# Kernel optimization log

Measured on AMD Instinct MI355X. Metric: run time of the kernel, lower is better.

The kernel has to match this reference:

```python
import jax, jax.numpy as jnp
import numpy as np

EPS = 1e-12

def gcn_layer(x, W, row, col, vals, n_nodes):
    # support = x @ W ; out = relu(spmm(adj, support)) with adj in COO form
    support = x @ W                                  # [N, out]
    msgs = vals[:, None] * support[col]              # [E, out] gather
    agg = jax.ops.segment_sum(msgs, row, num_segments=n_nodes)
    return jax.nn.relu(agg)

def l2norm(x):
    return x / jnp.maximum(jnp.linalg.norm(x, axis=1, keepdims=True), EPS)

def setup_inputs() -> dict:
    key = jax.random.key(0)
    ks = jax.random.split(key, 16)
    N, D, A, Da, E = 20000, 1000, 1000, 100, 160000
    inp = {
        'emb_sr': jax.random.normal(ks[0], (N, D), jnp.float32) * 0.02,
        'emb_tg': jax.random.normal(ks[1], (N, D), jnp.float32) * 0.02,
        'attr_weight_sr': jax.random.uniform(ks[2], (N, A), jnp.float32),
        'attr_weight_tg': jax.random.uniform(ks[3], (N, A), jnp.float32),
        'row_sr': jax.random.randint(ks[4], (E,), 0, N, jnp.int32),
        'col_sr': jax.random.randint(ks[5], (E,), 0, N, jnp.int32),
        'vals_sr': jax.random.uniform(ks[6], (E,), jnp.float32),
        'row_tg': jax.random.randint(ks[7], (E,), 0, N, jnp.int32),
        'col_tg': jax.random.randint(ks[8], (E,), 0, N, jnp.int32),
        'vals_tg': jax.random.uniform(ks[9], (E,), jnp.float32),
        'W_s0': jax.random.normal(ks[10], (D, D), jnp.float32) * (1.0 / np.sqrt(D)),
        'W_s1': jax.random.normal(ks[11], (D, D), jnp.float32) * (1.0 / np.sqrt(D)),
        'W_a11': jax.random.normal(ks[12], (A, Da), jnp.float32) * (1.0 / np.sqrt(A)),
        'W_a12': jax.random.normal(ks[13], (A, Da), jnp.float32) * (1.0 / np.sqrt(A)),
        'W_a2': jax.random.normal(ks[14], (Da, Da), jnp.float32) * (1.0 / np.sqrt(Da)),
    }
    return inp

def reference(emb_sr, emb_tg, attr_weight_sr, attr_weight_tg,
              row_sr, col_sr, vals_sr, row_tg, col_tg, vals_tg,
              W_s0, W_s1, W_a11, W_a12, W_a2):
    N = emb_sr.shape[0]
    M = emb_tg.shape[0]
    # structural branch: 2 shared GCN layers over each graph
    sr = emb_sr
    tg = emb_tg
    for W in (W_s0, W_s1):
        sr = gcn_layer(sr, W, row_sr, col_sr, vals_sr, N)
        tg = gcn_layer(tg, W, row_tg, col_tg, vals_tg, M)
    sr = l2norm(sr)
    tg = l2norm(tg)
    # attribute branch
    sr_a = gcn_layer(attr_weight_sr, W_a11, row_sr, col_sr, vals_sr, N)
    sr_a = gcn_layer(sr_a, W_a2, row_sr, col_sr, vals_sr, N)
    tg_a = gcn_layer(attr_weight_tg, W_a12, row_tg, col_tg, vals_tg, M)
    tg_a = gcn_layer(tg_a, W_a2, row_tg, col_tg, vals_tg, M)
    return (sr, tg, sr_a, tg_a)
```

## Files before the change

kernel.cpp:

```cpp
#include <hip/hip_runtime.h>

#define N_NODES 20000
#define D_IN    1000
#define E_EDGES 160000
#define DA      100

#define MPAD 20224
#define DP   1024
#define DAP  128
#define MBLK 157
#define NRB  1250
#define PEMAX (E_EDGES + 4 * N_NODES)

typedef __bf16 bf16x8 __attribute__((ext_vector_type(8)));
typedef float  f32x4  __attribute__((ext_vector_type(4)));
typedef short  short8v __attribute__((ext_vector_type(8)));

__device__ __forceinline__ short f2bf(float f) {
  __bf16 h = (__bf16)f;
  return *(short*)&h;
}
__device__ __forceinline__ float bf2f(short s) {
  return __uint_as_float(((unsigned)(unsigned short)s) << 16);
}

#define GLDS16(g, l) __builtin_amdgcn_global_load_lds( \
    (const __attribute__((address_space(1))) void*)(g), \
    (__attribute__((address_space(3))) void*)(l), 16, 0, 0)


__global__ void cvt_pad4_v3(const float* __restrict__ s0, const float* __restrict__ s1,
                            const float* __restrict__ s2, const float* __restrict__ s3,
                            short* __restrict__ d0, short* __restrict__ d1,
                            short* __restrict__ d2, short* __restrict__ d3) {
  const float* src; short* dst;
  switch (blockIdx.z) {
    case 0:  src = s0; dst = d0; break;
    case 1:  src = s1; dst = d1; break;
    case 2:  src = s2; dst = d2; break;
    default: src = s3; dst = d3; break;
  }
  const int lane = threadIdx.x & 63;
  const int r = blockIdx.y * 4 + (threadIdx.x >> 6);
  const int u1 = lane + 64;
  short8v o0 = {0, 0, 0, 0, 0, 0, 0, 0};
  short8v o1 = {0, 0, 0, 0, 0, 0, 0, 0};
  if (r < N_NODES) {
    const float* p0 = src + (size_t)r * D_IN + lane * 8;
    float4 a0 = *(const float4*)p0;
    float4 a1 = *(const float4*)(p0 + 4);
    o0[0] = f2bf(a0.x); o0[1] = f2bf(a0.y); o0[2] = f2bf(a0.z); o0[3] = f2bf(a0.w);
    o0[4] = f2bf(a1.x); o0[5] = f2bf(a1.y); o0[6] = f2bf(a1.z); o0[7] = f2bf(a1.w);
    if (u1 < 125) {
      const float* p1 = src + (size_t)r * D_IN + u1 * 8;
      float4 b0 = *(const float4*)p1;
      float4 b1 = *(const float4*)(p1 + 4);
      o1[0] = f2bf(b0.x); o1[1] = f2bf(b0.y); o1[2] = f2bf(b0.z); o1[3] = f2bf(b0.w);
      o1[4] = f2bf(b1.x); o1[5] = f2bf(b1.y); o1[6] = f2bf(b1.z); o1[7] = f2bf(b1.w);
    }
  }
  *(short8v*)&dst[(size_t)r * DP + lane * 8] = o0;
  *(short8v*)&dst[(size_t)r * DP + u1 * 8] = o1;
}

__global__ void cvt_w_t2_k(const float* __restrict__ s0, const float* __restrict__ s1,
                           int K, int Nc,
                           short* __restrict__ d0, short* __restrict__ d1, int Kp) {
  const float* src = blockIdx.z ? s1 : s0;
  short* dst = blockIdx.z ? d1 : d0;
  int n = blockIdx.y;
  int k = blockIdx.x * blockDim.x + threadIdx.x;
  if (k >= Kp) return;
  float v = (k < K && n < Nc) ? src[(size_t)k * Nc + n] : 0.f;
  dst[(size_t)n * Kp + k] = f2bf(v);
}

__global__ void zero_int_k(int* p, int n) {
  int i = blockIdx.x * blockDim.x + threadIdx.x;
  if (i < n) p[i] = 0;
}


__global__ void hist2_k(const int* __restrict__ row0, const int* __restrict__ row1, int E,
                        int* __restrict__ deg0, int* __restrict__ deg1) {
  int e = blockIdx.x * blockDim.x + threadIdx.x;
  if (e < E) atomicAdd(&deg0[row0[e]], 1);
  else if (e < 2 * E) atomicAdd(&deg1[row1[e - E]], 1);
}

#define SCAN_T 1024
#define SCAN_C 20
__launch_bounds__(SCAN_T)
__global__ void scan_pad2_k(const int* __restrict__ dg0, const int* __restrict__ dg1, int n,
                            int* __restrict__ p0, int* __restrict__ p1) {
  const int* deg = blockIdx.x ? dg1 : dg0;
  int* poffs = blockIdx.x ? p1 : p0;
  __shared__ int lds[SCAN_T];
  int t = threadIdx.x;
  int base = t * SCAN_C;
  int v[SCAN_C];
  int s = 0;
#pragma unroll
  for (int i = 0; i < SCAN_C; ++i) {
    int idx = base + i;
    int x = (idx < n) ? ((deg[idx] + 3) & ~3) : 0;
    s += x;
    v[i] = s;
  }
  lds[t] = s;
  __syncthreads();
  for (int off = 1; off < SCAN_T; off <<= 1) {
    int add = (t >= off) ? lds[t - off] : 0;
    __syncthreads();
    lds[t] += add;
    __syncthreads();
  }
  int prefix = lds[t] - s;
#pragma unroll
  for (int i = 0; i < SCAN_C; ++i) {
    int idx = base + i;
    if (idx < n) poffs[idx + 1] = v[i] + prefix;
  }
  if (t == 0) poffs[0] = 0;
}

__global__ void scatter_pack2_k(const int* __restrict__ row0, const int* __restrict__ col0,
                                const float* __restrict__ val0,
                                const int* __restrict__ row1, const int* __restrict__ col1,
                                const float* __restrict__ val1, int E,
                                const int* __restrict__ po0, const int* __restrict__ po1,
                                int* __restrict__ cur0, int* __restrict__ cur1,
                                int2* __restrict__ pk0, int2* __restrict__ pk1) {
  int e = blockIdx.x * blockDim.x + threadIdx.x;
  if (e < E) {
    int r = row0[e];
    int p = atomicAdd(&cur0[r], 1);
    pk0[po0[r] + p] = make_int2(col0[e], __float_as_int(val0[e]));
  } else if (e < 2 * E) {
    int ee = e - E;
    int r = row1[ee];
    int p = atomicAdd(&cur1[r], 1);
    pk1[po1[r] + p] = make_int2(col1[ee], __float_as_int(val1[ee]));
  }
}

__launch_bounds__(512, 1)
__global__ void gemm8p_k(const short* __restrict__ A0, const short* __restrict__ A1, int lda,
                         const short* __restrict__ Bt0, const short* __restrict__ Bt1, int ldb,
                         short* __restrict__ C0, short* __restrict__ C1, int ldc,
                         int nbCol, int nbRow) {
  __shared__ short lds[8][8192];

  int orig = blockIdx.x;
  int nwg = gridDim.x;
  int q = nwg >> 3, rr = nwg & 7;
  int xcd = orig & 7, idx = orig >> 3;
  int wg = (xcd < rr ? xcd * (q + 1) : rr * (q + 1) + (xcd - rr) * q) + idx;
  int colB = wg % nbCol;
  int t2 = wg / nbCol;
  int rowB = t2 % nbRow;
  int z = t2 / nbRow;

  const short* A  = z ? A1 : A0;
  const short* Bt = z ? Bt1 : Bt0;
  short* C        = z ? C1 : C0;

  const int tid  = threadIdx.x;
  const int lane = tid & 63;
  const int wid  = tid >> 6;
  const int wm   = wid >> 2;
  const int wn   = wid & 3;
  const int rowBase = rowB * 256;
  const int colBase = colB * 256;

  const int sC = (lane & 3) ^ ((lane >> 3) & 3);
  const short* baseA = A  + (size_t)(rowBase + wid * 32 + (lane >> 2)) * lda + sC * 8;
  const short* baseB = Bt + (size_t)(colBase + wid * 32 + (lane >> 2)) * ldb + sC * 8;

  const int chunkR = (lane >> 4) ^ ((lane >> 1) & 3);
  const int offA = (wm * 128 + (lane & 15)) * 32 + chunkR * 8;
  const int offB = (wn * 64  + (lane & 15)) * 32 + chunkR * 8;

  f32x4 acc[8][4];
#pragma unroll
  for (int m = 0; m < 8; ++m)
#pragma unroll
    for (int n = 0; n < 4; ++n)
      acc[m][n] = (f32x4){0.f, 0.f, 0.f, 0.f};

#define STAGE_HALF(h) do { \
    int tt_ = (h) >> 2; \
    int kc_ = tt_ * 64 + (((h) >> 1) & 1) * 32; \
    short* dst_ = &lds[(h) & 7][wid * 1024]; \
    if ((h) & 1) { GLDS16(baseB + kc_, dst_); GLDS16(baseB + kc_ + 16 * ldb, dst_ + 512); } \
    else         { GLDS16(baseA + kc_, dst_); GLDS16(baseA + kc_ + 16 * lda, dst_ + 512); } \
  } while (0)

  STAGE_HALF(0); STAGE_HALF(1); STAGE_HALF(2); STAGE_HALF(3); STAGE_HALF(4);
  asm volatile("s_waitcnt vmcnt(6)" ::: "memory");
  __builtin_amdgcn_s_barrier();

  bf16x8 bv[4];
  for (int t = 0; t < 16; ++t) {
    const int s0 = (4 * t) & 7;
    const int s1 = (4 * t + 2) & 7;

    {
      const short* pA = &lds[s0][0];
      const short* pB = &lds[s0 + 1][0];
      bf16x8 af[4];
#pragma unroll
      for (int n = 0; n < 4; ++n) bv[n] = *(const bf16x8*)&pB[offB + n * 512];
#pragma unroll
      for (int m = 0; m < 4; ++m) af[m] = *(const bf16x8*)&pA[offA + m * 512];
      { int h = 4 * t + 5; if (h < 64) STAGE_HALF(h); }
      __builtin_amdgcn_s_barrier();
      __builtin_amdgcn_s_setprio(1);
#pragma unroll
      for (int m = 0; m < 4; ++m)
#pragma unroll
        for (int n = 0; n < 4; ++n)
          acc[m][n] = __builtin_amdgcn_mfma_f32_16x16x32_bf16(af[m], bv[n], acc[m][n], 0, 0, 0);
      __builtin_amdgcn_s_setprio(0);
      __builtin_amdgcn_s_barrier();
    }
    {
      const short* pA = &lds[s0][0];
      bf16x8 af[4];
#pragma unroll
      for (int m = 0; m < 4; ++m) af[m] = *(const bf16x8*)&pA[offA + (4 + m) * 512];
      { int h = 4 * t + 6; if (h < 64) STAGE_HALF(h); }
      __builtin_amdgcn_s_barrier();
      __builtin_amdgcn_s_setprio(1);
#pragma unroll
      for (int m = 0; m < 4; ++m)
#pragma unroll
        for (int n = 0; n < 4; ++n)
          acc[4 + m][n] = __builtin_amdgcn_mfma_f32_16x16x32_bf16(af[m], bv[n], acc[4 + m][n], 0, 0, 0);
      __builtin_amdgcn_s_setprio(0);
      if (t < 15) { asm volatile("s_waitcnt vmcnt(6)" ::: "memory"); }
      else        { asm volatile("s_waitcnt vmcnt(0)" ::: "memory"); }
      __builtin_amdgcn_s_barrier();
    }
    {
      const short* pA = &lds[s1][0];
      const short* pB = &lds[s1 + 1][0];
      bf16x8 af[4];
#pragma unroll
      for (int n = 0; n < 4; ++n) bv[n] = *(const bf16x8*)&pB[offB + n * 512];
#pragma unroll
      for (int m = 0; m < 4; ++m) af[m] = *(const bf16x8*)&pA[offA + m * 512];
      { int h = 4 * t + 7; if (h < 64) STAGE_HALF(h); }
      __builtin_amdgcn_s_barrier();
      __builtin_amdgcn_s_setprio(1);
#pragma unroll
      for (int m = 0; m < 4; ++m)
#pragma unroll
        for (int n = 0; n < 4; ++n)
          acc[m][n] = __builtin_amdgcn_mfma_f32_16x16x32_bf16(af[m], bv[n], acc[m][n], 0, 0, 0);
      __builtin_amdgcn_s_setprio(0);
      __builtin_amdgcn_s_barrier();
    }
    {
      const short* pA = &lds[s1][0];
      bf16x8 af[4];
#pragma unroll
      for (int m = 0; m < 4; ++m) af[m] = *(const bf16x8*)&pA[offA + (4 + m) * 512];
      { int h = 4 * t + 8; if (h < 64) STAGE_HALF(h); }
      __builtin_amdgcn_s_barrier();
      __builtin_amdgcn_s_setprio(1);
#pragma unroll
      for (int m = 0; m < 4; ++m)
#pragma unroll
        for (int n = 0; n < 4; ++n)
          acc[4 + m][n] = __builtin_amdgcn_mfma_f32_16x16x32_bf16(af[m], bv[n], acc[4 + m][n], 0, 0, 0);
      __builtin_amdgcn_s_setprio(0);
      if (t < 14)       { asm volatile("s_waitcnt vmcnt(6)" ::: "memory"); }
      else if (t == 14) { asm volatile("s_waitcnt vmcnt(4)" ::: "memory"); }
      __builtin_amdgcn_s_barrier();
    }
  }
#undef STAGE_HALF

#pragma unroll
  for (int gm = 0; gm < 8; ++gm) {
#pragma unroll
    for (int n = 0; n < 4; ++n) {
      int r0 = rowBase + wm * 128 + gm * 16 + (lane >> 4) * 4;
      int c  = colBase + wn * 64 + n * 16 + (lane & 15);
#pragma unroll
      for (int reg = 0; reg < 4; ++reg)
        C[(size_t)(r0 + reg) * ldc + c] = f2bf(acc[gm][n][reg]);
    }
  }
}

__launch_bounds__(256, 2)
__global__ void gemm_bf16_k(const short* __restrict__ A0, const short* __restrict__ A1, int lda,
                            const short* __restrict__ Bt0, const short* __restrict__ Bt1, int ldb,
                            short* __restrict__ C0, short* __restrict__ C1, int ldc, int K,
                            int nbCol, int nbRow) {
  __shared__ short As[128 * 64];
  __shared__ short Bs[128 * 64];

  int orig = blockIdx.x;
  int nwg = gridDim.x;
  int q = nwg >> 3, rr = nwg & 7;
  int xcd = orig & 7, idx = orig >> 3;
  int wg = (xcd < rr ? xcd * (q + 1) : rr * (q + 1) + (xcd - rr) * q) + idx;
  int colB = wg % nbCol;
  int t2   = wg / nbCol;
  int rowB = t2 % nbRow;
  int z    = t2 / nbRow;

  const short* A  = z ? A1 : A0;
  const short* Bt = z ? Bt1 : Bt0;
  short* C        = z ? C1 : C0;

  const int tid  = threadIdx.x;
  const int lane = tid & 63;
  const int wid  = tid >> 6;
  const int wr   = wid >> 1;
  const int wc   = wid & 1;
  const int rowBase = rowB * 128;
  const int colBase = colB * 128;

  const int lrow = lane >> 3;
  const int kofs = (lane & 7) * 8;

  f32x4 acc[4][4];
#pragma unroll
  for (int m = 0; m < 4; ++m)
#pragma unroll
    for (int n = 0; n < 4; ++n)
      acc[m][n] = (f32x4){0.f, 0.f, 0.f, 0.f};

  for (int k0 = 0; k0 < K; k0 += 64) {
#pragma unroll
    for (int c = 0; c < 4; ++c) {
      int chunk = wid * 4 + c;
      int r = chunk * 8 + lrow;
      const short* g = A + (size_t)(rowBase + r) * lda + k0 + kofs;
      GLDS16(g, &As[chunk * 8 * 64]);
    }
#pragma unroll
    for (int c = 0; c < 4; ++c) {
      int chunk = wid * 4 + c;
      int r = chunk * 8 + lrow;
      const short* g = Bt + (size_t)(colBase + r) * ldb + k0 + kofs;
      GLDS16(g, &Bs[chunk * 8 * 64]);
    }
    __syncthreads();

    bf16x8 af[2][4], bfr[2][4];
#pragma unroll
    for (int kk = 0; kk < 2; ++kk) {
#pragma unroll
      for (int i = 0; i < 4; ++i) {
        int ar = wr * 64 + i * 16 + (lane & 15);
        af[kk][i]  = *(const bf16x8*)&As[ar * 64 + kk * 32 + (lane >> 4) * 8];
        int br = wc * 64 + i * 16 + (lane & 15);
        bfr[kk][i] = *(const bf16x8*)&Bs[br * 64 + kk * 32 + (lane >> 4) * 8];
      }
    }
#pragma unroll
    for (int kk = 0; kk < 2; ++kk)
#pragma unroll
      for (int m = 0; m < 4; ++m)
#pragma unroll
        for (int n = 0; n < 4; ++n)
          acc[m][n] = __builtin_amdgcn_mfma_f32_16x16x32_bf16(
              af[kk][m], bfr[kk][n], acc[m][n], 0, 0, 0);
    __syncthreads();
  }

#pragma unroll
  for (int m = 0; m < 4; ++m) {
#pragma unroll
    for (int n = 0; n < 4; ++n) {
      int row0 = rowBase + wr * 64 + m * 16 + (lane >> 4) * 4;
      int col  = colBase + wc * 64 + n * 16 + (lane & 15);
#pragma unroll
      for (int reg = 0; reg < 4; ++reg)
        C[(size_t)(row0 + reg) * ldc + col] = f2bf(acc[m][n][reg]);
    }
  }
}

template<int NCHUNK, int MODE>
__launch_bounds__(256)
__global__ void spmm_v5(const int* __restrict__ po0, const int* __restrict__ po1,
                        const int2* __restrict__ pk0, const int2* __restrict__ pk1,
                        const short* __restrict__ S0, const short* __restrict__ S1, int ldS,
                        short* __restrict__ oB0, short* __restrict__ oB1, int ldB,
                        float* __restrict__ oF0, float* __restrict__ oF1, int outCols) {
  int orig = blockIdx.x;
  int chunk, graph, rowBlk;
  if (NCHUNK == 8) {
    chunk = orig & 7;
    int idx = orig >> 3;
    graph = idx / NRB;
    rowBlk = idx - graph * NRB;
  } else {
    chunk = 0;
    graph = orig / NRB;
    rowBlk = orig - graph * NRB;
  }
  const int* poffs   = graph ? po1 : po0;
  const int2* packed = graph ? pk1 : pk0;
  const short* S     = graph ? S1 : S0;
  short* outB        = graph ? oB1 : oB0;
  float* outF        = graph ? oF1 : oF0;

  const int lane16 = threadIdx.x & 15;
  const int rowloc = threadIdx.x >> 4;
  const int r  = rowBlk * 16 + rowloc;
  const int c0 = chunk * 128 + lane16 * 8;

  int e0 = poffs[r], e1 = poffs[r + 1];
  float acc[8];
#pragma unroll
  for (int j = 0; j < 8; ++j) acc[j] = 0.f;

  for (int i = e0; i < e1; i += 4) {
    const int4* p4 = (const int4*)&packed[i];
    int4 a = p4[0];
    int4 b = p4[1];
    short8v s0 = *(const short8v*)&S[(size_t)a.x * ldS + c0];
    short8v s1 = *(const short8v*)&S[(size_t)a.z * ldS + c0];
    short8v s2 = *(const short8v*)&S[(size_t)b.x * ldS + c0];
    short8v s3 = *(const short8v*)&S[(size_t)b.z * ldS + c0];
    float v0 = __int_as_float(a.y);
    float v1 = __int_as_float(a.w);
    float v2 = __int_as_float(b.y);
    float v3 = __int_as_float(b.w);
#pragma unroll
    for (int j = 0; j < 8; ++j) {
      acc[j] += v0 * bf2f(s0[j]);
      acc[j] += v1 * bf2f(s1[j]);
      acc[j] += v2 * bf2f(s2[j]);
      acc[j] += v3 * bf2f(s3[j]);
    }
  }
#pragma unroll
  for (int j = 0; j < 8; ++j) acc[j] = fmaxf(acc[j], 0.f);

  if (MODE == 0) {
    short8v o;
#pragma unroll
    for (int j = 0; j < 8; ++j) o[j] = f2bf(acc[j]);
    *(short8v*)&outB[(size_t)r * ldB + c0] = o;
  } else {
#pragma unroll
    for (int j = 0; j < 8; ++j)
      if (c0 + j < outCols)
        outF[(size_t)r * outCols + c0 + j] = acc[j];
  }
}

__launch_bounds__(256)
__global__ void l2norm2_k(const short* __restrict__ H0, const short* __restrict__ H1, int ldH,
                          float* __restrict__ o0, float* __restrict__ o1, int cols) {
  const short* H = blockIdx.y ? H1 : H0;
  float* out = blockIdx.y ? o1 : o0;
  __shared__ float red[4];
  int r = blockIdx.x;
  int t = threadIdx.x;
  short4 v = ((const short4*)(H + (size_t)r * ldH))[t];
  float f0 = bf2f(v.x), f1 = bf2f(v.y), f2 = bf2f(v.z), f3 = bf2f(v.w);
  float s = f0 * f0 + f1 * f1 + f2 * f2 + f3 * f3;
  for (int off = 32; off >= 1; off >>= 1) s += __shfl_down(s, off, 64);
  if ((t & 63) == 0) red[t >> 6] = s;
  __syncthreads();
  float tot = red[0] + red[1] + red[2] + red[3];
  float inv = 1.f / fmaxf(sqrtf(tot), 1e-12f);
  int c0 = t * 4;
  float vals[4] = {f0, f1, f2, f3};
#pragma unroll
  for (int j = 0; j < 4; ++j)
    if (c0 + j < cols)
      out[(size_t)r * cols + c0 + j] = vals[j] * inv;
}


extern "C" void kernel_launch(void* const* d_in, const int* in_sizes, int n_in,
                              void* d_out, int out_size, void* d_ws, size_t ws_size,
                              hipStream_t stream) {
  const float* emb_sr  = (const float*)d_in[0];
  const float* emb_tg  = (const float*)d_in[1];
  const float* attr_sr = (const float*)d_in[2];
  const float* attr_tg = (const float*)d_in[3];
  const int*   row_sr  = (const int*)d_in[4];
  const int*   col_sr  = (const int*)d_in[5];
  const float* vals_sr = (const float*)d_in[6];
  const int*   row_tg  = (const int*)d_in[7];
  const int*   col_tg  = (const int*)d_in[8];
  const float* vals_tg = (const float*)d_in[9];
  const float* W_s0    = (const float*)d_in[10];
  const float* W_s1    = (const float*)d_in[11];
  const float* W_a11   = (const float*)d_in[12];
  const float* W_a12   = (const float*)d_in[13];
  const float* W_a2    = (const float*)d_in[14];

  const int N = N_NODES, Dd = D_IN, E = E_EDGES;

  char* ws = (char*)d_ws;
  size_t off = 0;
  auto alloc = [&](size_t bytes) -> void* {
    void* p = ws + off;
    off += (bytes + 255) & ~(size_t)255;
    return p;
  };
  short* X0 = (short*)alloc((size_t)MPAD * DP * 2);
  short* X1 = (short*)alloc((size_t)MPAD * DP * 2);
  short* T0 = (short*)alloc((size_t)MPAD * DP * 2);
  short* T1 = (short*)alloc((size_t)MPAD * DP * 2);
  short* Y0 = (short*)alloc((size_t)MPAD * DP * 2);
  short* Y1 = (short*)alloc((size_t)MPAD * DP * 2);
  short* Ws0t  = (short*)alloc((size_t)DP * DP * 2);
  short* Ws1t  = (short*)alloc((size_t)DP * DP * 2);
  short* Wa11t = (short*)alloc((size_t)DAP * DP * 2);
  short* Wa12t = (short*)alloc((size_t)DAP * DP * 2);
  short* Wa2t  = (short*)alloc((size_t)DAP * DAP * 2);
  int*  ibuf    = (int*)alloc((size_t)4 * N * 4);
  int2* pack_sr = (int2*)alloc((size_t)PEMAX * 8);
  int2* pack_tg = (int2*)alloc((size_t)PEMAX * 8);
  int*  poffs_sr = (int*)alloc((size_t)(N + 1) * 4);
  int*  poffs_tg = (int*)alloc((size_t)(N + 1) * 4);
  if (off > ws_size) return;

  int* deg_sr = ibuf;
  int* cur_sr = ibuf + N;
  int* deg_tg = ibuf + 2 * N;
  int* cur_tg = ibuf + 3 * N;
  const int ZERO_N = 4 * N + 2 * (PEMAX * 2);

  float* out_sr  = (float*)d_out;
  float* out_tg  = out_sr + (size_t)N * Dd;
  float* out_sra = out_tg + (size_t)N * Dd;
  float* out_tga = out_sra + (size_t)N * DA;

  zero_int_k<<<dim3((ZERO_N + 255) / 256), 256, 0, stream>>>(ibuf, ZERO_N);
  hist2_k<<<dim3((2 * E + 255) / 256), 256, 0, stream>>>(row_sr, row_tg, E, deg_sr, deg_tg);
  scan_pad2_k<<<2, SCAN_T, 0, stream>>>(deg_sr, deg_tg, N, poffs_sr, poffs_tg);
  scatter_pack2_k<<<dim3((2 * E + 255) / 256), 256, 0, stream>>>(
      row_sr, col_sr, vals_sr, row_tg, col_tg, vals_tg, E,
      poffs_sr, poffs_tg, cur_sr, cur_tg, pack_sr, pack_tg);

  cvt_pad4_v3<<<dim3(1, MPAD / 4, 4), 256, 0, stream>>>(emb_sr, emb_tg, attr_sr, attr_tg,
                                                        X0, X1, Y0, Y1);
  cvt_w_t2_k<<<dim3(DP / 256, DP, 2), 256, 0, stream>>>(W_s0, W_s1, Dd, Dd, Ws0t, Ws1t, DP);
  cvt_w_t2_k<<<dim3(DP / 256, DAP, 2), 256, 0, stream>>>(W_a11, W_a12, Dd, DA, Wa11t, Wa12t, DP);
  cvt_w_t2_k<<<dim3(1, DAP, 1), 256, 0, stream>>>(W_a2, W_a2, DA, DA, Wa2t, Wa2t, DAP);

  gemm8p_k<<<dim3(79 * 4 * 2), 512, 0, stream>>>(X0, X1, DP, Ws0t, Ws0t, DP,
                                                 T0, T1, DP, 4, 79);
  spmm_v5<8, 0><<<dim3(8 * 2 * NRB), 256, 0, stream>>>(
      poffs_sr, poffs_tg, pack_sr, pack_tg, T0, T1, DP, X0, X1, DP, nullptr, nullptr, 0);
  gemm8p_k<<<dim3(79 * 4 * 2), 512, 0, stream>>>(X0, X1, DP, Ws1t, Ws1t, DP,
                                                 T0, T1, DP, 4, 79);
  spmm_v5<8, 0><<<dim3(8 * 2 * NRB), 256, 0, stream>>>(
      poffs_sr, poffs_tg, pack_sr, pack_tg, T0, T1, DP, X0, X1, DP, nullptr, nullptr, 0);
  l2norm2_k<<<dim3(N, 2), 256, 0, stream>>>(X0, X1, DP, out_sr, out_tg, Dd);

  gemm_bf16_k<<<dim3(1 * MBLK * 2), 256, 0, stream>>>(Y0, Y1, DP, Wa11t, Wa12t, DP,
                                                      T0, T1, DAP, DP, 1, MBLK);
  spmm_v5<1, 0><<<dim3(2 * NRB), 256, 0, stream>>>(
      poffs_sr, poffs_tg, pack_sr, pack_tg, T0, T1, DAP, X0, X1, DAP, nullptr, nullptr, 0);
  gemm_bf16_k<<<dim3(1 * MBLK * 2), 256, 0, stream>>>(X0, X1, DAP, Wa2t, Wa2t, DAP,
                                                      T0, T1, DAP, DAP, 1, MBLK);
  spmm_v5<1, 1><<<dim3(2 * NRB), 256, 0, stream>>>(
      poffs_sr, poffs_tg, pack_sr, pack_tg, T0, T1, DAP, nullptr, nullptr, 0, out_sra, out_tga, DA);
}
```

Baseline: 642.4 us.

## Shrink big GEMM tile to 128x256 with 4-stage uniform K pipeline

Replaces the 256x256-tile, 8-slot half-step pipelined GEMM with a 128x256 tile that loads A and B together per 32-wide K step into a 4-deep LDS ring, prefetching three steps ahead. This doubles the grid (158 row blocks per graph) so more workgroups can be spread across CUs for the 20224x1024 problem, and it simplifies the schedule. The trade-off is lower arithmetic intensity per tile, since each B tile is reloaded twice as often, and a finer sync cadence with a barrier pair every K step.

```diff
diff --git a/kernel.cpp b/kernel.cpp
--- a/kernel.cpp
+++ b/kernel.cpp
@@ -9,6 +9,7 @@
 #define DP   1024
 #define DAP  128
 #define MBLK 157
+#define NBR8 158
 #define NRB  1250
 #define PEMAX (E_EDGES + 4 * N_NODES)
 
@@ -145,11 +146,12 @@
 }
 
 __launch_bounds__(512, 1)
-__global__ void gemm8p_k(const short* __restrict__ A0, const short* __restrict__ A1, int lda,
-                         const short* __restrict__ Bt0, const short* __restrict__ Bt1, int ldb,
-                         short* __restrict__ C0, short* __restrict__ C1, int ldc,
-                         int nbCol, int nbRow) {
-  __shared__ short lds[8][8192];
+__global__ void gemm8p2_k(const short* __restrict__ A0, const short* __restrict__ A1, int lda,
+                          const short* __restrict__ Bt0, const short* __restrict__ Bt1, int ldb,
+                          short* __restrict__ C0, short* __restrict__ C1, int ldc,
+                          int nbCol, int nbRow) {
+  __shared__ short sA[4][4096];
+  __shared__ short sB[4][8192];
 
   int orig = blockIdx.x;
   int nwg = gridDim.x;
@@ -170,127 +172,79 @@
   const int wid  = tid >> 6;
   const int wm   = wid >> 2;
   const int wn   = wid & 3;
-  const int rowBase = rowB * 256;
+  const int rowBase = rowB * 128;
   const int colBase = colB * 256;
 
   const int sC = (lane & 3) ^ ((lane >> 3) & 3);
-  const short* baseA = A  + (size_t)(rowBase + wid * 32 + (lane >> 2)) * lda + sC * 8;
-  const short* baseB = Bt + (size_t)(colBase + wid * 32 + (lane >> 2)) * ldb + sC * 8;
-
-  const int chunkR = (lane >> 4) ^ ((lane >> 1) & 3);
-  const int offA = (wm * 128 + (lane & 15)) * 32 + chunkR * 8;
-  const int offB = (wn * 64  + (lane & 15)) * 32 + chunkR * 8;
-
-  f32x4 acc[8][4];
-#pragma unroll
-  for (int m = 0; m < 8; ++m)
+  const short* baseA  = A  + (size_t)(rowBase + wid * 16 + (lane >> 2)) * lda + sC * 8;
+  const short* baseB0 = Bt + (size_t)(colBase + wid * 16 + (lane >> 2)) * ldb + sC * 8;
+  const short* baseB1 = Bt + (size_t)(colBase + 128 + wid * 16 + (lane >> 2)) * ldb + sC * 8;
+
+  int offA[4], offB[4];
+#pragma unroll
+  for (int m = 0; m < 4; ++m) {
+    int row = wm * 64 + m * 16 + (lane & 15);
+    int ch = (lane >> 4) ^ ((row >> 1) & 3);
+    offA[m] = row * 32 + ch * 8;
+  }
+#pragma unroll
+  for (int n = 0; n < 4; ++n) {
+    int row = wn * 64 + n * 16 + (lane & 15);
+    int ch = (lane >> 4) ^ ((row >> 1) & 3);
+    offB[n] = row * 32 + ch * 8;
+  }
+
+  f32x4 acc[4][4];
+#pragma unroll
+  for (int m = 0; m < 4; ++m)
 #pragma unroll
     for (int n = 0; n < 4; ++n)
       acc[m][n] = (f32x4){0.f, 0.f, 0.f, 0.f};
 
-#define STAGE_HALF(h) do { \
-    int tt_ = (h) >> 2; \
-    int kc_ = tt_ * 64 + (((h) >> 1) & 1) * 32; \
-    short* dst_ = &lds[(h) & 7][wid * 1024]; \
-    if ((h) & 1) { GLDS16(baseB + kc_, dst_); GLDS16(baseB + kc_ + 16 * ldb, dst_ + 512); } \
-    else         { GLDS16(baseA + kc_, dst_); GLDS16(baseA + kc_ + 16 * lda, dst_ + 512); } \
+#define STAGE_P(p) do { \
+    int kc_ = (p) * 32; \
+    GLDS16(baseA  + kc_, &sA[(p) & 3][wid * 512]); \
+    GLDS16(baseB0 + kc_, &sB[(p) & 3][wid * 512]); \
+    GLDS16(baseB1 + kc_, &sB[(p) & 3][4096 + wid * 512]); \
   } while (0)
 
-  STAGE_HALF(0); STAGE_HALF(1); STAGE_HALF(2); STAGE_HALF(3); STAGE_HALF(4);
+  STAGE_P(0); STAGE_P(1); STAGE_P(2);
   asm volatile("s_waitcnt vmcnt(6)" ::: "memory");
   __builtin_amdgcn_s_barrier();
 
-  bf16x8 bv[4];
-  for (int t = 0; t < 16; ++t) {
-    const int s0 = (4 * t) & 7;
-    const int s1 = (4 * t + 2) & 7;
-
-    {
-      const short* pA = &lds[s0][0];
-      const short* pB = &lds[s0 + 1][0];
-      bf16x8 af[4];
-#pragma unroll
-      for (int n = 0; n < 4; ++n) bv[n] = *(const bf16x8*)&pB[offB + n * 512];
-#pragma unroll
-      for (int m = 0; m < 4; ++m) af[m] = *(const bf16x8*)&pA[offA + m * 512];
-      { int h = 4 * t + 5; if (h < 64) STAGE_HALF(h); }
-      __builtin_amdgcn_s_barrier();
-      __builtin_amdgcn_s_setprio(1);
-#pragma unroll
-      for (int m = 0; m < 4; ++m)
-#pragma unroll
-        for (int n = 0; n < 4; ++n)
-          acc[m][n] = __builtin_amdgcn_mfma_f32_16x16x32_bf16(af[m], bv[n], acc[m][n], 0, 0, 0);
-      __builtin_amdgcn_s_setprio(0);
-      __builtin_amdgcn_s_barrier();
-    }
-    {
-      const short* pA = &lds[s0][0];
-      bf16x8 af[4];
-#pragma unroll
-      for (int m = 0; m < 4; ++m) af[m] = *(const bf16x8*)&pA[offA + (4 + m) * 512];
-      { int h = 4 * t + 6; if (h < 64) STAGE_HALF(h); }
-      __builtin_amdgcn_s_barrier();
-      __builtin_amdgcn_s_setprio(1);
-#pragma unroll
-      for (int m = 0; m < 4; ++m)
-#pragma unroll
-        for (int n = 0; n < 4; ++n)
-          acc[4 + m][n] = __builtin_amdgcn_mfma_f32_16x16x32_bf16(af[m], bv[n], acc[4 + m][n], 0, 0, 0);
-      __builtin_amdgcn_s_setprio(0);
-      if (t < 15) { asm volatile("s_waitcnt vmcnt(6)" ::: "memory"); }
-      else        { asm volatile("s_waitcnt vmcnt(0)" ::: "memory"); }
-      __builtin_amdgcn_s_barrier();
-    }
-    {
-      const short* pA = &lds[s1][0];
-      const short* pB = &lds[s1 + 1][0];
-      bf16x8 af[4];
-#pragma unroll
-      for (int n = 0; n < 4; ++n) bv[n] = *(const bf16x8*)&pB[offB + n * 512];
-#pragma unroll
-      for (int m = 0; m < 4; ++m) af[m] = *(const bf16x8*)&pA[offA + m * 512];
-      { int h = 4 * t + 7; if (h < 64) STAGE_HALF(h); }
-      __builtin_amdgcn_s_barrier();
-      __builtin_amdgcn_s_setprio(1);
-#pragma unroll
-      for (int m = 0; m < 4; ++m)
-#pragma unroll
-        for (int n = 0; n < 4; ++n)
-          acc[m][n] = __builtin_amdgcn_mfma_f32_16x16x32_bf16(af[m], bv[n], acc[m][n], 0, 0, 0);
-      __builtin_amdgcn_s_setprio(0);
-      __builtin_amdgcn_s_barrier();
-    }
-    {
-      const short* pA = &lds[s1][0];
-      bf16x8 af[4];
-#pragma unroll
-      for (int m = 0; m < 4; ++m) af[m] = *(const bf16x8*)&pA[offA + (4 + m) * 512];
-      { int h = 4 * t + 8; if (h < 64) STAGE_HALF(h); }
-      __builtin_amdgcn_s_barrier();
-      __builtin_amdgcn_s_setprio(1);
-#pragma unroll
-      for (int m = 0; m < 4; ++m)
-#pragma unroll
-        for (int n = 0; n < 4; ++n)
-          acc[4 + m][n] = __builtin_amdgcn_mfma_f32_16x16x32_bf16(af[m], bv[n], acc[4 + m][n], 0, 0, 0);
-      __builtin_amdgcn_s_setprio(0);
-      if (t < 14)       { asm volatile("s_waitcnt vmcnt(6)" ::: "memory"); }
-      else if (t == 14) { asm volatile("s_waitcnt vmcnt(4)" ::: "memory"); }
-      __builtin_amdgcn_s_barrier();
-    }
-  }
-#undef STAGE_HALF
-
-#pragma unroll
-  for (int gm = 0; gm < 8; ++gm) {
+  for (int p = 0; p < 32; ++p) {
+    const short* pA = &sA[p & 3][0];
+    const short* pB = &sB[p & 3][0];
+    bf16x8 af[4], bv[4];
+#pragma unroll
+    for (int m = 0; m < 4; ++m) af[m] = *(const bf16x8*)&pA[offA[m]];
+#pragma unroll
+    for (int n = 0; n < 4; ++n) bv[n] = *(const bf16x8*)&pB[offB[n]];
+    if (p < 29) STAGE_P(p + 3);
+    __builtin_amdgcn_s_barrier();
+    __builtin_amdgcn_s_setprio(1);
+#pragma unroll
+    for (int m = 0; m < 4; ++m)
+#pragma unroll
+      for (int n = 0; n < 4; ++n)
+        acc[m][n] = __builtin_amdgcn_mfma_f32_16x16x32_bf16(af[m], bv[n], acc[m][n], 0, 0, 0);
+    __builtin_amdgcn_s_setprio(0);
+    if (p < 29)       { asm volatile("s_waitcnt vmcnt(6)" ::: "memory"); }
+    else if (p == 29) { asm volatile("s_waitcnt vmcnt(3)" ::: "memory"); }
+    else if (p == 30) { asm volatile("s_waitcnt vmcnt(0)" ::: "memory"); }
+    __builtin_amdgcn_s_barrier();
+  }
+#undef STAGE_P
+
+#pragma unroll
+  for (int m = 0; m < 4; ++m) {
 #pragma unroll
     for (int n = 0; n < 4; ++n) {
-      int r0 = rowBase + wm * 128 + gm * 16 + (lane >> 4) * 4;
+      int r0 = rowBase + wm * 64 + m * 16 + (lane >> 4) * 4;
       int c  = colBase + wn * 64 + n * 16 + (lane & 15);
 #pragma unroll
       for (int reg = 0; reg < 4; ++reg)
-        C[(size_t)(r0 + reg) * ldc + c] = f2bf(acc[gm][n][reg]);
+        C[(size_t)(r0 + reg) * ldc + c] = f2bf(acc[m][n][reg]);
     }
   }
 }
@@ -553,12 +507,12 @@
   cvt_w_t2_k<<<dim3(DP / 256, DAP, 2), 256, 0, stream>>>(W_a11, W_a12, Dd, DA, Wa11t, Wa12t, DP);
   cvt_w_t2_k<<<dim3(1, DAP, 1), 256, 0, stream>>>(W_a2, W_a2, DA, DA, Wa2t, Wa2t, DAP);
 
-  gemm8p_k<<<dim3(79 * 4 * 2), 512, 0, stream>>>(X0, X1, DP, Ws0t, Ws0t, DP,
-                                                 T0, T1, DP, 4, 79);
+  gemm8p2_k<<<dim3(NBR8 * 4 * 2), 512, 0, stream>>>(X0, X1, DP, Ws0t, Ws0t, DP,
+                                                    T0, T1, DP, 4, NBR8);
   spmm_v5<8, 0><<<dim3(8 * 2 * NRB), 256, 0, stream>>>(
       poffs_sr, poffs_tg, pack_sr, pack_tg, T0, T1, DP, X0, X1, DP, nullptr, nullptr, 0);
-  gemm8p_k<<<dim3(79 * 4 * 2), 512, 0, stream>>>(X0, X1, DP, Ws1t, Ws1t, DP,
-                                                 T0, T1, DP, 4, 79);
+  gemm8p2_k<<<dim3(NBR8 * 4 * 2), 512, 0, stream>>>(X0, X1, DP, Ws1t, Ws1t, DP,
+                                                    T0, T1, DP, 4, NBR8);
   spmm_v5<8, 0><<<dim3(8 * 2 * NRB), 256, 0, stream>>>(
       poffs_sr, poffs_tg, pack_sr, pack_tg, T0, T1, DP, X0, X1, DP, nullptr, nullptr, 0);
   l2norm2_k<<<dim3(N, 2), 256, 0, stream>>>(X0, X1, DP, out_sr, out_tg, Dd);
```

New measurement: 679.3 us. +5.7%, slower.
